# Performance work log

Measured on AMD Instinct MI355X. Metric: run time of the kernel, lower is better.

The kernel has to match this reference:

```python
import jax, jax.numpy as jnp
import numpy as np

M, NQ, NKV, DX, DT = 8, 1024, 1024, 512, 2
H, HD = 8, 64            # num_heads, head_dim
INNER = H * HD           # 512
KHID = 16                # kernel MLP hidden dim
SCALE = HD ** -0.5


def setup_inputs() -> dict:
    key = jax.random.key(0)
    ks = jax.random.split(key, 16)
    s = lambda fan_in: 1.0 / np.sqrt(fan_in)
    return {
        "xq": jax.random.normal(ks[0], (M, NQ, DX), jnp.float32),
        "xk": jax.random.normal(ks[1], (M, NKV, DX), jnp.float32),
        "xv": jax.random.normal(ks[2], (M, NKV, DX), jnp.float32),
        "tq": jax.random.normal(ks[3], (M, NQ, DT), jnp.float32),
        "tk": jax.random.normal(ks[4], (M, NKV, DT), jnp.float32),
        # attention projections (bias=False for q/k/v, Linear bias for out)
        "w_q": jax.random.normal(ks[5], (DX, INNER), jnp.float32) * s(DX),
        "w_k": jax.random.normal(ks[6], (DX, INNER), jnp.float32) * s(DX),
        "w_v": jax.random.normal(ks[7], (DX, INNER), jnp.float32) * s(DX),
        "w_out": jax.random.normal(ks[8], (INNER, DX), jnp.float32) * s(INNER),
        "b_out": jnp.zeros((DX,), jnp.float32),
        # kernel MLP: dt -> KHID -> H (per-head pairwise bias)
        "kw1": jax.random.normal(ks[9], (DT, KHID), jnp.float32) * s(DT),
        "kb1": jnp.zeros((KHID,), jnp.float32),
        "kw2": jax.random.normal(ks[10], (KHID, H), jnp.float32) * s(KHID),
        "kb2": jnp.zeros((H,), jnp.float32),
    }


def reference(xq, xk, xv, tq, tk, w_q, w_k, w_v, w_out, b_out, kw1, kb1, kw2, kb2):
    # pairwise differences of input locations: [m, nq, nkv, dt]
    diff = tq[:, :, None, :] - tk[:, None, :, :]
    # kernel MLP -> per-head bias, rearranged to [m, h, nq, nkv]
    hmid = jax.nn.relu(diff @ kw1 + kb1)          # [m, nq, nkv, KHID]
    dots = jnp.einsum('mqkc,ch->mhqk', hmid, kw2) + kb2[None, :, None, None]
    # token attention: standard scaled QK scores
    q = (xq @ w_q).reshape(M, NQ, H, HD)          # [m, nq, h, d]
    k = (xk @ w_k).reshape(M, NKV, H, HD)
    token_dots = jnp.einsum('mqhd,mkhd->mhqk', q, k) * SCALE
    dots = dots + token_dots
    attn = jax.nn.softmax(dots, axis=-1)          # softmax over keys
    v = (xv @ w_v).reshape(M, NKV, H, HD)
    out = jnp.einsum('mhqk,mkhd->mqhd', attn, v).reshape(M, NQ, INNER)
    return out @ w_out + b_out                    # [m, nq, dx]
```

## Files before the change

### kernel.cpp

```cpp
#include <hip/hip_runtime.h>


typedef unsigned short u16;
typedef unsigned int   u32;
typedef short bf8 __attribute__((ext_vector_type(8)));
typedef float f4  __attribute__((ext_vector_type(4)));
typedef _Float16 h2 __attribute__((ext_vector_type(2)));

#define Mb 8
#define SCALE 0.125f
#define NTOK 4194304

__device__ __forceinline__ u16 f2bf(float f) {
    union { float f; u32 u; } v; v.f = f;
    u32 r = v.u + 0x7fffu + ((v.u >> 16) & 1u);
    return (u16)(r >> 16);
}
__device__ __forceinline__ u32 pk2(float a, float b) {
    u32 r;
    asm("v_cvt_pk_bf16_f32 %0, %1, %2" : "=v"(r) : "v"(a), "v"(b));
    return r;
}
__device__ __forceinline__ void gl_lds16(const u16* g, u16* l) {
    __builtin_amdgcn_global_load_lds(
        (const __attribute__((address_space(1))) u32*)g,
        (__attribute__((address_space(3))) u32*)l, 16, 0, 0);
}
__device__ __forceinline__ h2 h2_of(u32 x) {
    union { u32 u; h2 h; } c; c.u = x; return c.h;
}
__device__ __forceinline__ u32 u_of(h2 x) {
    union { h2 h; u32 u; } c; c.h = x; return c.u;
}
__device__ __forceinline__ float dot2(h2 a, h2 b, float c) {
#if __has_builtin(__builtin_amdgcn_fdot2)
    return __builtin_amdgcn_fdot2(a, b, c, false);
#else
    return fmaf((float)a[0], (float)b[0], fmaf((float)a[1], (float)b[1], c));
#endif
}

struct PArgs {
    const float* xs[3];
    const float* ws[4];
    u16* dstA;
    u16* dstW;
};

__global__ __launch_bounds__(256) void prep(PArgs p) {
    __shared__ u16 tl[64][80];
    const int tid = threadIdx.x;
    const int b = blockIdx.x;
    if (b < 1536) {
        #pragma unroll
        for (int it = 0; it < 4; ++it) {
            const u32 u = (u32)b * 256u + (u32)tid + (u32)it * 393216u;
            const int arr = u >> 19;
            const size_t off = (size_t)(u & 524287u) * 8;
            const float* s = p.xs[arr];
            float4 a0 = *(const float4*)(s + off);
            float4 a1 = *(const float4*)(s + off + 4);
            uint4 v;
            v.x = pk2(a0.x, a0.y); v.y = pk2(a0.z, a0.w);
            v.z = pk2(a1.x, a1.y); v.w = pk2(a1.z, a1.w);
            *(uint4*)(p.dstA + (size_t)arr * NTOK + off) = v;
        }
    } else {
        const int bb = b - 1536;
        const int mat = bb >> 6, t = bb & 63;
        const int kt = t >> 3, nt = t & 7;
        const float* src = p.ws[mat] + (size_t)kt * 64 * 512 + (size_t)nt * 64;
        const int r0 = tid >> 4, c4 = (tid & 15) * 4;
        #pragma unroll
        for (int rr = 0; rr < 4; ++rr) {
            const int row = r0 + rr * 16;
            float4 a = *(const float4*)(src + (size_t)row * 512 + c4);
            tl[c4 + 0][row] = f2bf(a.x);
            tl[c4 + 1][row] = f2bf(a.y);
            tl[c4 + 2][row] = f2bf(a.z);
            tl[c4 + 3][row] = f2bf(a.w);
        }
        __syncthreads();
        u16* dst = p.dstW + (size_t)mat * 262144 + (size_t)nt * 64 * 512 + (size_t)kt * 64;
        #pragma unroll
        for (int i = 0; i < 2; ++i) {
            const int s2 = tid + i * 256;
            const int nrow = s2 >> 3, k8 = (s2 & 7) * 8;
            *(uint4*)(dst + (size_t)nrow * 512 + k8) = *(const uint4*)&tl[nrow][k8];
        }
    }
}

struct GArgs {
    const u16*   A[3];
    const u16*   W[3];
    void*        C[3];
    const float* bias;
    int          modeT[3];
    int          outf32;
};

__global__ __launch_bounds__(256) void gemm_mfma(GArgs g) {
    __shared__ u16 Xs[128][32];
    __shared__ u16 Ws[128][32];

    const int z   = blockIdx.z;
    const int tid = threadIdx.x;
    const int w = tid >> 6, lane = tid & 63, quad = lane >> 4, l16 = lane & 15;
    const int wm = w >> 1, wn = w & 1;
    const int n0 = blockIdx.x * 128, t0 = blockIdx.y * 128;
    const int trans = g.modeT[z];

    f4 acc[4][4];
    #pragma unroll
    for (int i = 0; i < 4; ++i)
        #pragma unroll
        for (int j = 0; j < 4; ++j) acc[i][j] = (f4)0.f;

    const int lrow  = lane >> 2;
    const int kslot = (lane & 3) ^ ((lane >> 3) & 3);
    u16* ldsX0 = &Xs[w * 32][0];
    u16* ldsX1 = &Xs[w * 32 + 16][0];
    u16* ldsW0 = &Ws[w * 32][0];
    u16* ldsW1 = &Ws[w * 32 + 16][0];
    const u16* gA0 = g.A[z] + (size_t)(t0 + w * 32 + lrow) * 512 + kslot * 8;
    const u16* gA1 = gA0 + 16 * 512;
    const u16* gW0 = g.W[z] + (size_t)(n0 + w * 32 + lrow) * 512 + kslot * 8;
    const u16* gW1 = gW0 + 16 * 512;

    const int rslot = (quad ^ ((l16 >> 1) & 3)) * 8;

    for (int kc = 0; kc < 512; kc += 32) {
        __syncthreads();
        gl_lds16(gA0 + kc, ldsX0);
        gl_lds16(gA1 + kc, ldsX1);
        gl_lds16(gW0 + kc, ldsW0);
        gl_lds16(gW1 + kc, ldsW1);
        __syncthreads();

        const u16* Abase = trans ? &Xs[0][0] : &Ws[0][0];
        const u16* Bbase = trans ? &Ws[0][0] : &Xs[0][0];
        const int arow = (trans ? wm : wn) * 64;
        const int brow = (trans ? wn : wm) * 64;
        bf8 af[4], bf[4];
        #pragma unroll
        for (int i = 0; i < 4; ++i)
            af[i] = *(const bf8*)(Abase + (arow + i * 16 + l16) * 32 + rslot);
        #pragma unroll
        for (int j = 0; j < 4; ++j)
            bf[j] = *(const bf8*)(Bbase + (brow + j * 16 + l16) * 32 + rslot);
        #pragma unroll
        for (int i = 0; i < 4; ++i)
            #pragma unroll
            for (int j = 0; j < 4; ++j)
                acc[i][j] = __builtin_amdgcn_mfma_f32_16x16x32_bf16(af[i], bf[j], acc[i][j], 0, 0, 0);
    }

    if (g.outf32) {
        float* Co = (float*)g.C[z];
        #pragma unroll
        for (int i = 0; i < 4; ++i) {
            const int nb = n0 + wn * 64 + i * 16 + quad * 4;
            float4 bv = *(const float4*)&g.bias[nb];
            #pragma unroll
            for (int j = 0; j < 4; ++j) {
                const int tok = t0 + wm * 64 + j * 16 + l16;
                float4 st;
                st.x = acc[i][j][0] + bv.x; st.y = acc[i][j][1] + bv.y;
                st.z = acc[i][j][2] + bv.z; st.w = acc[i][j][3] + bv.w;
                *(float4*)&Co[(size_t)tok * 512 + nb] = st;
            }
        }
    } else if (!trans) {
        u16* C = (u16*)g.C[z];
        #pragma unroll
        for (int i = 0; i < 4; ++i) {
            const int nb = n0 + wn * 64 + i * 16 + quad * 4;
            #pragma unroll
            for (int j = 0; j < 4; ++j) {
                const int tok = t0 + wm * 64 + j * 16 + l16;
                uint2 pw;
                pw.x = pk2(acc[i][j][0], acc[i][j][1]);
                pw.y = pk2(acc[i][j][2], acc[i][j][3]);
                *(uint2*)&C[(size_t)tok * 512 + nb] = pw;
            }
        }
    } else {
        u16* Vt = (u16*)g.C[z];
        #pragma unroll
        for (int i = 0; i < 4; ++i) {
            const int tokb = t0 + wm * 64 + i * 16 + quad * 4;
            const int mb = tokb >> 10, tb = tokb & 1023;
            #pragma unroll
            for (int j = 0; j < 4; ++j) {
                const int n = n0 + wn * 64 + j * 16 + l16;
                uint2 pw;
                pw.x = pk2(acc[i][j][0], acc[i][j][1]);
                pw.y = pk2(acc[i][j][2], acc[i][j][3]);
                *(uint2*)&Vt[(size_t)mb * 524288 + (size_t)n * 1024 + tb] = pw;
            }
        }
    }
}

__global__ __launch_bounds__(512) void attn_mfma(
    const u16* __restrict__ Q, const u16* __restrict__ K,
    const u16* __restrict__ Vt,
    const float* __restrict__ tqp, const float* __restrict__ tkp,
    const float* __restrict__ kw1, const float* __restrict__ kb1,
    const float* __restrict__ kw2,
    u16* __restrict__ O)
{
    __shared__ u16 sK[2][8][64][8];
    __shared__ u16 sV[2][8][64][8];
    __shared__ u32 sv2[2][8][68];
    __shared__ u16 sP[8][16][68];

    const int tid = threadIdx.x;
    const int w = tid >> 6, lane = tid & 63, quad = lane >> 4, l16 = lane & 15;
    const int b = (blockIdx.z * 8 + blockIdx.y) * 8 + blockIdx.x;
    const int xc = b & 7, j = b >> 3;
    const int hm = xc * 8 + (j & 7);
    const int qt = j >> 3;
    const int h = hm & 7, m = hm >> 3;
    const int q0 = qt * 128;
    const size_t qtok = (size_t)m * 1024 + q0 + w * 16 + l16;

    bf8 qf[2];
    {
        const u16* qp = Q + qtok * 512 + h * 64 + quad * 8;
        qf[0] = *(const bf8*)qp;
        qf[1] = *(const bf8*)(qp + 32);
    }
    h2 u2[8], w2p[8];
    {
        const float t0v = tqp[qtok * 2], t1v = tqp[qtok * 2 + 1];
        #pragma unroll
        for (int cp = 0; cp < 8; ++cp) {
            const int c0 = 2 * cp, c1 = 2 * cp + 1;
            float ua = fmaf(t0v, kw1[c0], fmaf(t1v, kw1[16 + c0], kb1[c0]));
            float ub = fmaf(t0v, kw1[c1], fmaf(t1v, kw1[16 + c1], kb1[c1]));
            u2[cp][0]  = (_Float16)ua;              u2[cp][1]  = (_Float16)ub;
            w2p[cp][0] = (_Float16)kw2[c0 * 8 + h]; w2p[cp][1] = (_Float16)kw2[c1 * 8 + h];
        }
    }
    const float w0a = kw1[2 * w],     w1a = kw1[16 + 2 * w];
    const float w0b = kw1[2 * w + 1], w1b = kw1[16 + 2 * w + 1];

    const u16* gK = K + ((size_t)m * 1024 + lane) * 512 + h * 64 + w * 8;
    const u16* gV = Vt + (size_t)m * 524288 + (size_t)(h * 64 + lane) * 1024 + w * 8;
    const float* gT = tkp + (size_t)m * 2048 + lane * 2;

    float mrun = -1e30f, lrun = 0.f;
    f4 o[4];
    #pragma unroll
    for (int d = 0; d < 4; ++d) o[d] = (f4)0.f;

    auto STAGE = [&](int kt2, int nb) {
        const int k0n = kt2 * 64;
        float2 t = *(const float2*)(gT + k0n * 2);
        h2 pv;
        pv[0] = (_Float16)fmaf(t.x, w0a, t.y * w1a);
        pv[1] = (_Float16)fmaf(t.x, w0b, t.y * w1b);
        sv2[nb][w][lane] = u_of(pv);
        gl_lds16(gK + (size_t)k0n * 512, &sK[nb][w][0][0]);
        gl_lds16(gV + k0n,               &sV[nb][w][0][0]);
    };

    STAGE(0, 0);
    __syncthreads();

    int cur = 0;
    for (int kt = 0; kt < 16; ++kt) {
        if (kt < 15) STAGE(kt + 1, cur ^ 1);

        f4 s[4];
        #pragma unroll
        for (int msub = 0; msub < 4; ++msub) {
            bf8 kf0 = *(const bf8*)&sK[cur][quad][msub * 16 + l16][0];
            bf8 kf1 = *(const bf8*)&sK[cur][4 + quad][msub * 16 + l16][0];
            s[msub] = __builtin_amdgcn_mfma_f32_16x16x32_bf16(kf0, qf[0], (f4)0.f, 0, 0, 0);
            s[msub] = __builtin_amdgcn_mfma_f32_16x16x32_bf16(kf1, qf[1], s[msub], 0, 0, 0);
        }
        #pragma unroll
        for (int msub = 0; msub < 4; ++msub) {
            const int kb = msub * 16 + quad * 4;
            f4 b2 = (f4)0.f;
            #pragma unroll
            for (int cp = 0; cp < 8; ++cp) {
                uint4 vv = *(const uint4*)&sv2[cur][cp][kb];
                const h2 uc = u2[cp], wc = w2p[cp];
                const h2 z = (h2)(_Float16)0.f;
                h2 d0 = uc - h2_of(vv.x);
                h2 d1 = uc - h2_of(vv.y);
                h2 d2 = uc - h2_of(vv.z);
                h2 d3 = uc - h2_of(vv.w);
                d0 = __builtin_elementwise_max(d0, z);
                d1 = __builtin_elementwise_max(d1, z);
                d2 = __builtin_elementwise_max(d2, z);
                d3 = __builtin_elementwise_max(d3, z);
                b2[0] = dot2(d0, wc, b2[0]);
                b2[1] = dot2(d1, wc, b2[1]);
                b2[2] = dot2(d2, wc, b2[2]);
                b2[3] = dot2(d3, wc, b2[3]);
            }
            s[msub] = s[msub] * SCALE + b2;
        }
        float mx = -1e30f;
        #pragma unroll
        for (int msub = 0; msub < 4; ++msub) {
            mx = fmaxf(mx, fmaxf(fmaxf(s[msub][0], s[msub][1]),
                                 fmaxf(s[msub][2], s[msub][3])));
        }
        mx = fmaxf(mx, __shfl_xor(mx, 16));
        mx = fmaxf(mx, __shfl_xor(mx, 32));
        const float mnew = fmaxf(mrun, mx);
        float ps = 0.f;
        #pragma unroll
        for (int msub = 0; msub < 4; ++msub) {
            #pragma unroll
            for (int r = 0; r < 4; ++r) {
                float p = __expf(s[msub][r] - mnew);
                s[msub][r] = p;
                ps += p;
            }
        }
        ps += __shfl_xor(ps, 16);
        ps += __shfl_xor(ps, 32);
        if (__all(mx <= mrun)) {
            lrun += ps;
        } else {
            const float alpha = __expf(mrun - mnew);
            lrun = lrun * alpha + ps;
            mrun = mnew;
            #pragma unroll
            for (int d = 0; d < 4; ++d) o[d] = o[d] * alpha;
        }
        #pragma unroll
        for (int msub = 0; msub < 4; ++msub) {
            uint2 pw;
            pw.x = pk2(s[msub][0], s[msub][1]);
            pw.y = pk2(s[msub][2], s[msub][3]);
            *(uint2*)&sP[w][l16][msub * 16 + quad * 4] = pw;
        }
        #pragma unroll
        for (int dsub = 0; dsub < 4; ++dsub) {
            #pragma unroll
            for (int kc2 = 0; kc2 < 2; ++kc2) {
                bf8 vf = *(const bf8*)&sV[cur][kc2 * 4 + quad][dsub * 16 + l16][0];
                bf8 pf = *(const bf8*)&sP[w][l16][kc2 * 32 + quad * 8];
                o[dsub] = __builtin_amdgcn_mfma_f32_16x16x32_bf16(vf, pf, o[dsub], 0, 0, 0);
            }
        }

        if (kt < 15) __syncthreads();
        cur ^= 1;
    }

    const float inv = 1.f / lrun;
    #pragma unroll
    for (int dsub = 0; dsub < 4; ++dsub) {
        uint2 pw;
        pw.x = pk2(o[dsub][0] * inv, o[dsub][1] * inv);
        pw.y = pk2(o[dsub][2] * inv, o[dsub][3] * inv);
        *(uint2*)&O[qtok * 512 + h * 64 + dsub * 16 + quad * 4] = pw;
    }
}

extern "C" void kernel_launch(void* const* d_in, const int* in_sizes, int n_in,
                              void* d_out, int out_size, void* d_ws, size_t ws_size,
                              hipStream_t stream) {
    const float* xq    = (const float*)d_in[0];
    const float* xk    = (const float*)d_in[1];
    const float* xv    = (const float*)d_in[2];
    const float* tq    = (const float*)d_in[3];
    const float* tk    = (const float*)d_in[4];
    const float* w_q   = (const float*)d_in[5];
    const float* w_k   = (const float*)d_in[6];
    const float* w_v   = (const float*)d_in[7];
    const float* w_out = (const float*)d_in[8];
    const float* b_out = (const float*)d_in[9];
    const float* kw1   = (const float*)d_in[10];
    const float* kb1   = (const float*)d_in[11];
    const float* kw2   = (const float*)d_in[12];

    u16* Q  = (u16*)d_ws;
    u16* Kp = Q  + NTOK;
    u16* Vt = Kp + NTOK;
    u16* Aq = Vt + NTOK;
    u16* Ak = Aq + NTOK;
    u16* Av = Ak + NTOK;
    u16* Wq = Av + NTOK;
    u16* Wk = Wq + 262144;
    u16* Wv = Wk + 262144;
    u16* Wo = Wv + 262144;
    u16* O  = Aq;

    PArgs p;
    p.xs[0] = xq;  p.xs[1] = xk;  p.xs[2] = xv;
    p.ws[0] = w_q; p.ws[1] = w_k; p.ws[2] = w_v; p.ws[3] = w_out;
    p.dstA = Aq;   p.dstW = Wq;
    prep<<<dim3(1792), 256, 0, stream>>>(p);

    GArgs gq;
    gq.A[0] = Aq;  gq.A[1] = Ak;  gq.A[2] = Av;
    gq.W[0] = Wq;  gq.W[1] = Wk;  gq.W[2] = Wv;
    gq.C[0] = Q;   gq.C[1] = Kp;  gq.C[2] = Vt;
    gq.bias = nullptr;
    gq.modeT[0] = 0; gq.modeT[1] = 0; gq.modeT[2] = 1;
    gq.outf32 = 0;
    gemm_mfma<<<dim3(4, 64, 3), 256, 0, stream>>>(gq);

    attn_mfma<<<dim3(8, 8, Mb), 512, 0, stream>>>(Q, Kp, Vt, tq, tk,
                                                  kw1, kb1, kw2, O);

    GArgs go;
    go.A[0] = O;   go.A[1] = O;   go.A[2] = O;
    go.W[0] = Wo;  go.W[1] = Wo;  go.W[2] = Wo;
    go.C[0] = d_out; go.C[1] = d_out; go.C[2] = d_out;
    go.bias = b_out;
    go.modeT[0] = 0; go.modeT[1] = 0; go.modeT[2] = 0;
    go.outf32 = 1;
    gemm_mfma<<<dim3(4, 64, 1), 256, 0, stream>>>(go);
}
```

Baseline: 250.8 us.

## Fuse fp32-to-bf16 activation conversion into QKV GEMM and use exp2 softmax

The separate prep pass that converted xq/xk/xv to bf16 is removed. The QKV GEMM now loads fp32 activations directly, converts them in registers and stores them swizzled into LDS, which removes a full write and reread of three 16 MB bf16 buffers. The attention softmax folds log2(e) into the score scale and the kernel-MLP output weights so it can call exp2f instead of __expf. In exchange, each GEMM tile now rereads fp32 A data across the four N-blocks and converts it again, and the A load becomes a synchronous register path instead of a direct global-to-LDS load.

```diff
diff --git a/kernel.cpp b/kernel.cpp
--- a/kernel.cpp
+++ b/kernel.cpp
@@ -8,7 +8,8 @@
 typedef _Float16 h2 __attribute__((ext_vector_type(2)));
 
 #define Mb 8
-#define SCALE 0.125f
+#define LOG2E 1.44269504088896f
+#define SCALE2 (0.125f * LOG2E)
 #define NTOK 4194304
 
 __device__ __forceinline__ u16 f2bf(float f) {
@@ -41,63 +42,45 @@
 }
 
 struct PArgs {
-    const float* xs[3];
     const float* ws[4];
-    u16* dstA;
     u16* dstW;
 };
 
 __global__ __launch_bounds__(256) void prep(PArgs p) {
     __shared__ u16 tl[64][80];
     const int tid = threadIdx.x;
-    const int b = blockIdx.x;
-    if (b < 1536) {
-        #pragma unroll
-        for (int it = 0; it < 4; ++it) {
-            const u32 u = (u32)b * 256u + (u32)tid + (u32)it * 393216u;
-            const int arr = u >> 19;
-            const size_t off = (size_t)(u & 524287u) * 8;
-            const float* s = p.xs[arr];
-            float4 a0 = *(const float4*)(s + off);
-            float4 a1 = *(const float4*)(s + off + 4);
-            uint4 v;
-            v.x = pk2(a0.x, a0.y); v.y = pk2(a0.z, a0.w);
-            v.z = pk2(a1.x, a1.y); v.w = pk2(a1.z, a1.w);
-            *(uint4*)(p.dstA + (size_t)arr * NTOK + off) = v;
-        }
-    } else {
-        const int bb = b - 1536;
-        const int mat = bb >> 6, t = bb & 63;
-        const int kt = t >> 3, nt = t & 7;
-        const float* src = p.ws[mat] + (size_t)kt * 64 * 512 + (size_t)nt * 64;
-        const int r0 = tid >> 4, c4 = (tid & 15) * 4;
-        #pragma unroll
-        for (int rr = 0; rr < 4; ++rr) {
-            const int row = r0 + rr * 16;
-            float4 a = *(const float4*)(src + (size_t)row * 512 + c4);
-            tl[c4 + 0][row] = f2bf(a.x);
-            tl[c4 + 1][row] = f2bf(a.y);
-            tl[c4 + 2][row] = f2bf(a.z);
-            tl[c4 + 3][row] = f2bf(a.w);
-        }
-        __syncthreads();
-        u16* dst = p.dstW + (size_t)mat * 262144 + (size_t)nt * 64 * 512 + (size_t)kt * 64;
-        #pragma unroll
-        for (int i = 0; i < 2; ++i) {
-            const int s2 = tid + i * 256;
-            const int nrow = s2 >> 3, k8 = (s2 & 7) * 8;
-            *(uint4*)(dst + (size_t)nrow * 512 + k8) = *(const uint4*)&tl[nrow][k8];
-        }
+    const int bb = blockIdx.x;
+    const int mat = bb >> 6, t = bb & 63;
+    const int kt = t >> 3, nt = t & 7;
+    const float* src = p.ws[mat] + (size_t)kt * 64 * 512 + (size_t)nt * 64;
+    const int r0 = tid >> 4, c4 = (tid & 15) * 4;
+    #pragma unroll
+    for (int rr = 0; rr < 4; ++rr) {
+        const int row = r0 + rr * 16;
+        float4 a = *(const float4*)(src + (size_t)row * 512 + c4);
+        tl[c4 + 0][row] = f2bf(a.x);
+        tl[c4 + 1][row] = f2bf(a.y);
+        tl[c4 + 2][row] = f2bf(a.z);
+        tl[c4 + 3][row] = f2bf(a.w);
+    }
+    __syncthreads();
+    u16* dst = p.dstW + (size_t)mat * 262144 + (size_t)nt * 64 * 512 + (size_t)kt * 64;
+    #pragma unroll
+    for (int i = 0; i < 2; ++i) {
+        const int s2 = tid + i * 256;
+        const int nrow = s2 >> 3, k8 = (s2 & 7) * 8;
+        *(uint4*)(dst + (size_t)nrow * 512 + k8) = *(const uint4*)&tl[nrow][k8];
     }
 }
 
 struct GArgs {
-    const u16*   A[3];
+    const void*  A[3];
     const u16*   W[3];
     void*        C[3];
     const float* bias;
     int          modeT[3];
     int          outf32;
+    int          af32;
 };
 
 __global__ __launch_bounds__(256) void gemm_mfma(GArgs g) {
@@ -119,21 +102,41 @@
 
     const int lrow  = lane >> 2;
     const int kslot = (lane & 3) ^ ((lane >> 3) & 3);
+    u16* ldsW0 = &Ws[w * 32][0];
+    u16* ldsW1 = &Ws[w * 32 + 16][0];
+    const u16* gW0 = g.W[z] + (size_t)(n0 + w * 32 + lrow) * 512 + kslot * 8;
+    const u16* gW1 = gW0 + 16 * 512;
+
     u16* ldsX0 = &Xs[w * 32][0];
     u16* ldsX1 = &Xs[w * 32 + 16][0];
-    u16* ldsW0 = &Ws[w * 32][0];
-    u16* ldsW1 = &Ws[w * 32 + 16][0];
-    const u16* gA0 = g.A[z] + (size_t)(t0 + w * 32 + lrow) * 512 + kslot * 8;
+    const u16* gA0 = (const u16*)g.A[z] + (size_t)(t0 + w * 32 + lrow) * 512 + kslot * 8;
     const u16* gA1 = gA0 + 16 * 512;
-    const u16* gW0 = g.W[z] + (size_t)(n0 + w * 32 + lrow) * 512 + kslot * 8;
-    const u16* gW1 = gW0 + 16 * 512;
+    const int arow_s = tid >> 1, ah = tid & 1;
+    const float* aF = (const float*)g.A[z] + (size_t)(t0 + arow_s) * 512 + ah * 16;
+    const int s_sw = (arow_s >> 1) & 3;
+    u16* aw0 = &Xs[arow_s][((2 * ah)     ^ s_sw) * 8];
+    u16* aw1 = &Xs[arow_s][((2 * ah + 1) ^ s_sw) * 8];
 
     const int rslot = (quad ^ ((l16 >> 1) & 3)) * 8;
 
     for (int kc = 0; kc < 512; kc += 32) {
         __syncthreads();
-        gl_lds16(gA0 + kc, ldsX0);
-        gl_lds16(gA1 + kc, ldsX1);
+        if (g.af32) {
+            float4 f0 = *(const float4*)(aF + kc);
+            float4 f1 = *(const float4*)(aF + kc + 4);
+            float4 f2 = *(const float4*)(aF + kc + 8);
+            float4 f3 = *(const float4*)(aF + kc + 12);
+            uint4 v0, v1;
+            v0.x = pk2(f0.x, f0.y); v0.y = pk2(f0.z, f0.w);
+            v0.z = pk2(f1.x, f1.y); v0.w = pk2(f1.z, f1.w);
+            v1.x = pk2(f2.x, f2.y); v1.y = pk2(f2.z, f2.w);
+            v1.z = pk2(f3.x, f3.y); v1.w = pk2(f3.z, f3.w);
+            *(uint4*)aw0 = v0;
+            *(uint4*)aw1 = v1;
+        } else {
+            gl_lds16(gA0 + kc, ldsX0);
+            gl_lds16(gA1 + kc, ldsX1);
+        }
         gl_lds16(gW0 + kc, ldsW0);
         gl_lds16(gW1 + kc, ldsW1);
         __syncthreads();
@@ -240,8 +243,9 @@
             const int c0 = 2 * cp, c1 = 2 * cp + 1;
             float ua = fmaf(t0v, kw1[c0], fmaf(t1v, kw1[16 + c0], kb1[c0]));
             float ub = fmaf(t0v, kw1[c1], fmaf(t1v, kw1[16 + c1], kb1[c1]));
-            u2[cp][0]  = (_Float16)ua;              u2[cp][1]  = (_Float16)ub;
-            w2p[cp][0] = (_Float16)kw2[c0 * 8 + h]; w2p[cp][1] = (_Float16)kw2[c1 * 8 + h];
+            u2[cp][0]  = (_Float16)ua;  u2[cp][1]  = (_Float16)ub;
+            w2p[cp][0] = (_Float16)(LOG2E * kw2[c0 * 8 + h]);
+            w2p[cp][1] = (_Float16)(LOG2E * kw2[c1 * 8 + h]);
         }
     }
     const float w0a = kw1[2 * w],     w1a = kw1[16 + 2 * w];
@@ -304,7 +308,7 @@
                 b2[2] = dot2(d2, wc, b2[2]);
                 b2[3] = dot2(d3, wc, b2[3]);
             }
-            s[msub] = s[msub] * SCALE + b2;
+            s[msub] = s[msub] * SCALE2 + b2;
         }
         float mx = -1e30f;
         #pragma unroll
@@ -320,7 +324,7 @@
         for (int msub = 0; msub < 4; ++msub) {
             #pragma unroll
             for (int r = 0; r < 4; ++r) {
-                float p = __expf(s[msub][r] - mnew);
+                float p = exp2f(s[msub][r] - mnew);
                 s[msub][r] = p;
                 ps += p;
             }
@@ -330,7 +334,7 @@
         if (__all(mx <= mrun)) {
             lrun += ps;
         } else {
-            const float alpha = __expf(mrun - mnew);
+            const float alpha = exp2f(mrun - mnew);
             lrun = lrun * alpha + ps;
             mrun = mnew;
             #pragma unroll
@@ -387,28 +391,24 @@
     u16* Q  = (u16*)d_ws;
     u16* Kp = Q  + NTOK;
     u16* Vt = Kp + NTOK;
-    u16* Aq = Vt + NTOK;
-    u16* Ak = Aq + NTOK;
-    u16* Av = Ak + NTOK;
-    u16* Wq = Av + NTOK;
+    u16* O  = Vt + NTOK;
+    u16* Wq = O  + 3 * (size_t)NTOK;
     u16* Wk = Wq + 262144;
     u16* Wv = Wk + 262144;
     u16* Wo = Wv + 262144;
-    u16* O  = Aq;
 
     PArgs p;
-    p.xs[0] = xq;  p.xs[1] = xk;  p.xs[2] = xv;
     p.ws[0] = w_q; p.ws[1] = w_k; p.ws[2] = w_v; p.ws[3] = w_out;
-    p.dstA = Aq;   p.dstW = Wq;
-    prep<<<dim3(1792), 256, 0, stream>>>(p);
+    p.dstW = Wq;
+    prep<<<dim3(256), 256, 0, stream>>>(p);
 
     GArgs gq;
-    gq.A[0] = Aq;  gq.A[1] = Ak;  gq.A[2] = Av;
+    gq.A[0] = xq;  gq.A[1] = xk;  gq.A[2] = xv;
     gq.W[0] = Wq;  gq.W[1] = Wk;  gq.W[2] = Wv;
     gq.C[0] = Q;   gq.C[1] = Kp;  gq.C[2] = Vt;
     gq.bias = nullptr;
     gq.modeT[0] = 0; gq.modeT[1] = 0; gq.modeT[2] = 1;
-    gq.outf32 = 0;
+    gq.outf32 = 0; gq.af32 = 1;
     gemm_mfma<<<dim3(4, 64, 3), 256, 0, stream>>>(gq);
 
     attn_mfma<<<dim3(8, 8, Mb), 512, 0, stream>>>(Q, Kp, Vt, tq, tk,
@@ -420,6 +420,6 @@
     go.C[0] = d_out; go.C[1] = d_out; go.C[2] = d_out;
     go.bias = b_out;
     go.modeT[0] = 0; go.modeT[1] = 0; go.modeT[2] = 0;
-    go.outf32 = 1;
+    go.outf32 = 1; go.af32 = 0;
     gemm_mfma<<<dim3(4, 64, 1), 256, 0, stream>>>(go);
 }
```

Result: slower. 259.7 us (+3.6%).
